# Optimization experiments

Hardware: AMD Instinct MI355X
Metric: run time of the kernel (lower is better)

## Reference

```python
import jax, jax.numpy as jnp
import numpy as np

IN_SIZE = 96
HIDDEN = 128
LIN_IN = 32
T = 65536


def setup_inputs() -> dict:
    key = jax.random.key(0)
    ks = jax.random.split(key, 6)
    s_ih = 1.0 / np.sqrt(HIDDEN)
    return {
        "input_GRU": jax.random.normal(ks[0], (T, IN_SIZE), dtype=jnp.float32),
        "input_linear": jax.random.normal(ks[1], (T, LIN_IN), dtype=jnp.float32),
        "init_hidden": jnp.zeros((HIDDEN,), dtype=jnp.float32),
        "w_ih": (jax.random.normal(ks[2], (3 * HIDDEN, IN_SIZE), dtype=jnp.float32) * s_ih),
        "w_hh": (jax.random.normal(ks[3], (3 * HIDDEN, HIDDEN), dtype=jnp.float32) * s_ih),
        "b_ih": (jax.random.normal(ks[4], (3 * HIDDEN,), dtype=jnp.float32) * s_ih),
        "b_n": (jax.random.normal(ks[5], (HIDDEN,), dtype=jnp.float32) * s_ih),
        "lin_bias": jnp.zeros((1,), dtype=jnp.float32),
    }


def reference(input_GRU, input_linear, init_hidden, w_ih, w_hh, b_ih, b_n, lin_bias):
    # Precompute all input-to-hidden projections as one big GEMM: (T, 3H)
    igates_all = input_GRU @ w_ih.T + b_ih

    def step(h, inp):
        igates, x_lin = inp
        hgates = w_hh @ h  # (3H,)
        ir, iz, in_ = jnp.split(igates, 3)
        hr, hz, hn = jnp.split(hgates, 3)
        r = jax.nn.sigmoid(ir + hr)  # reset gate
        z = jax.nn.sigmoid(iz + hz)  # update gate
        n = jnp.tanh(in_ + r * (hn + b_n))  # candidate
        h_new = n + z * (h - n)  # equinox GRUCell update
        # dynamic linear readout: first LIN_IN hidden units act as weight row
        out = jnp.dot(h_new[:LIN_IN], x_lin)[None] + lin_bias  # (1,)
        return h_new, out

    _, out = jax.lax.scan(step, init_hidden, (igates_all, input_linear))
    return out  # (T, 1)
```

## Files before the change

### kernel.cpp

```cpp
#include <hip/hip_runtime.h>
#include <math.h>

#define IN_SIZE 96
#define HID 128
#define H3 384
#define LIN_IN 32

__global__ __launch_bounds__(384, 2)
void igates_kernel(const float* __restrict__ x, const float* __restrict__ w_ih,
                   const float* __restrict__ b_ih, float* __restrict__ ig, int T)
{
    const int TT = 16;
    int t0 = blockIdx.x * TT;
    int j = threadIdx.x;
    __shared__ __align__(16) float xs[TT * IN_SIZE];
    for (int idx = j; idx < TT * IN_SIZE; idx += H3)
        xs[idx] = x[(size_t)t0 * IN_SIZE + idx];
    __syncthreads();

    float acc[TT];
    float b = b_ih[j];
#pragma unroll
    for (int tt = 0; tt < TT; tt++) acc[tt] = b;

    const float4* w4 = (const float4*)(w_ih + (size_t)j * IN_SIZE);
#pragma unroll
    for (int k = 0; k < IN_SIZE / 4; k++) {
        float4 wv = w4[k];
#pragma unroll
        for (int tt = 0; tt < TT; tt++) {
            const float4* xv4 = (const float4*)(xs + tt * IN_SIZE);
            float4 xv = xv4[k];
            acc[tt] = fmaf(wv.x, xv.x, acc[tt]);
            acc[tt] = fmaf(wv.y, xv.y, acc[tt]);
            acc[tt] = fmaf(wv.z, xv.z, acc[tt]);
            acc[tt] = fmaf(wv.w, xv.w, acc[tt]);
        }
    }
#pragma unroll
    for (int tt = 0; tt < TT; tt++)
        ig[(size_t)(t0 + tt) * H3 + j] = acc[tt];
}

__device__ __forceinline__ void fma4(float4& acc, const float4& wv, const float4& hv)
{
    acc.x = fmaf(wv.x, hv.x, acc.x);
    acc.y = fmaf(wv.y, hv.y, acc.y);
    acc.z = fmaf(wv.z, hv.z, acc.z);
    acc.w = fmaf(wv.w, hv.w, acc.w);
}

__device__ __forceinline__ float quad_sum(float x)
{
    float t;
    t = __int_as_float(__builtin_amdgcn_mov_dpp(__float_as_int(x), 0xB1, 0xF, 0xF, true));
    x += t;
    t = __int_as_float(__builtin_amdgcn_mov_dpp(__float_as_int(x), 0x4E, 0xF, 0xF, true));
    x += t;
    return x;
}

__device__ __forceinline__ void fast_barrier()
{
    asm volatile("s_waitcnt lgkmcnt(0)\n\ts_barrier" ::: "memory");
}

#define HPAD 36

__global__
__attribute__((amdgpu_flat_work_group_size(512, 512), amdgpu_waves_per_eu(2, 2)))
void scan_kernel(const float* __restrict__ ig, const float* __restrict__ h0,
                 const float* __restrict__ w_hh, const float* __restrict__ b_n,
                 float* __restrict__ hlin, int T)
{
    __shared__ __align__(16) float hs[4 * HPAD];

    const int tid = threadIdx.x;
    const int j = tid >> 2;
    const int kseg = tid & 3;
    const bool gate_lane = (kseg == 0);

    float4 w0[8], w1[8], w2[8];
    {
        const float* b0 = w_hh + (size_t)j * HID + kseg * 32;
        const float* b1 = w_hh + (size_t)(j + HID) * HID + kseg * 32;
        const float* b2 = w_hh + (size_t)(j + 2 * HID) * HID + kseg * 32;
#pragma unroll
        for (int k = 0; k < 8; k++) {
            w0[k] = ((const float4*)b0)[k];
            w1[k] = ((const float4*)b1)[k];
            w2[k] = ((const float4*)b2)[k];
        }
    }
    if (tid < HID) hs[(tid >> 5) * HPAD + (tid & 31)] = h0[tid];

    float bn = 0.f;
    float p00 = 0.f, p01 = 0.f, p02 = 0.f;
    float p10 = 0.f, p11 = 0.f, p12 = 0.f;
    if (gate_lane) {
        bn = b_n[j];
        p00 = ig[j];
        p01 = ig[HID + j];
        p02 = ig[2 * HID + j];
        const float* q = ig + H3;
        p10 = q[j];
        p11 = q[HID + j];
        p12 = q[2 * HID + j];
    }
    __syncthreads();

    const float4* hp = (const float4*)(hs + kseg * HPAD);
    const int hwidx = (j >> 5) * HPAD + (j & 31);

    const float* pf = ig + (size_t)2 * H3 + j;
    float* hl = hlin + j;

#define MATVEC_GATES(C0, C1, C2, DO_PREFETCH)                                  \
    {                                                                          \
        float4 a0 = {0.f, 0.f, 0.f, 0.f}, a1 = a0, a2 = a0;                    \
        _Pragma("unroll")                                                      \
        for (int kk = 0; kk < 8; kk++) {                                       \
            float4 hv = hp[kk];                                                \
            fma4(a0, w0[kk], hv);                                              \
            fma4(a1, w1[kk], hv);                                              \
            fma4(a2, w2[kk], hv);                                              \
        }                                                                      \
        float s0 = (a0.x + a0.y) + (a0.z + a0.w);                              \
        float s1 = (a1.x + a1.y) + (a1.z + a1.w);                              \
        float s2 = (a2.x + a2.y) + (a2.z + a2.w);                              \
        s0 = quad_sum(s0); s1 = quad_sum(s1); s2 = quad_sum(s2);               \
        if (gate_lane) {                                                       \
            float hprev = hs[hwidx];                                           \
            float er = __expf(-(C0 + s0));                                     \
            float r = __builtin_amdgcn_rcpf(1.f + er);                         \
            float ez = __expf(-(C1 + s1));                                     \
            float z = __builtin_amdgcn_rcpf(1.f + ez);                         \
            float xn = C2 + r * (s2 + bn);                                     \
            float e2 = __expf(-2.f * fabsf(xn));                               \
            float th = (1.f - e2) * __builtin_amdgcn_rcpf(1.f + e2);           \
            float nn = copysignf(th, xn);                                      \
            float hnew = nn + z * (hprev - nn);                                \
            hs[hwidx] = hnew;                                                  \
            if (j < LIN_IN) *hl = hnew;                                        \
            if (DO_PREFETCH) {                 \
                C0 = pf[0];                                                    \
                C1 = pf[HID];                                                  \
                C2 = pf[2 * HID];                                              \
            }                                                                  \
        }                                                                      \
        hl += LIN_IN;                                                          \
        pf += H3;                                                              \
        fast_barrier();                                                        \
    }

    int s = 0;
    for (; s + 4 <= T; s += 2) {
        MATVEC_GATES(p00, p01, p02, true)
        MATVEC_GATES(p10, p11, p12, true)
    }
    MATVEC_GATES(p00, p01, p02, false)
    MATVEC_GATES(p10, p11, p12, false)
#undef MATVEC_GATES
}

__global__ __launch_bounds__(256)
void readout_kernel(const float* __restrict__ hlin, const float* __restrict__ xlin,
                    const float* __restrict__ lbias, float* __restrict__ out, int T)
{
    int gid = blockIdx.x * 256 + threadIdx.x;
    int t = gid >> 3;
    int seg = gid & 7;
    if (t < T) {
        float4 hv = ((const float4*)hlin)[(size_t)t * 8 + seg];
        float4 xv = ((const float4*)xlin)[(size_t)t * 8 + seg];
        float p = hv.x * xv.x + hv.y * xv.y + hv.z * xv.z + hv.w * xv.w;
        p += __shfl_xor(p, 1);
        p += __shfl_xor(p, 2);
        p += __shfl_xor(p, 4);
        if (seg == 0) out[t] = p + lbias[0];
    }
}

extern "C" void kernel_launch(void* const* d_in, const int* in_sizes, int n_in,
                              void* d_out, int out_size, void* d_ws, size_t ws_size,
                              hipStream_t stream) {
    const float* x_gru = (const float*)d_in[0];
    const float* x_lin = (const float*)d_in[1];
    const float* h0    = (const float*)d_in[2];
    const float* w_ih  = (const float*)d_in[3];
    const float* w_hh  = (const float*)d_in[4];
    const float* b_ih  = (const float*)d_in[5];
    const float* b_n   = (const float*)d_in[6];
    const float* lbias = (const float*)d_in[7];
    float* out = (float*)d_out;

    int T = in_sizes[0] / IN_SIZE;
    float* igates = (float*)d_ws;
    float* hlin   = (float*)d_ws + (size_t)T * H3;

    igates_kernel<<<T / 16, 384, 0, stream>>>(x_gru, w_ih, b_ih, igates, T);
    scan_kernel<<<1, 512, 0, stream>>>(igates, h0, w_hh, b_n, hlin, T);
    readout_kernel<<<(T * 8 + 255) / 256, 256, 0, stream>>>(hlin, x_lin, lbias, out, T);
}
```

Baseline: 31.92 ms.

## Halve scan workgroup to 256 threads, each handling two hidden units

The sequential GRU scan now runs with 256 threads (4 waves) instead of 512. Each quad of threads computes gates for two hidden units (g and g+64), holding twice as many w_hh registers. The aim is to cut the per-step barrier cost and wave count on the serial critical path. In exchange each thread does twice the FMAs per step, and register pressure rises to 192 floats of weights per thread, which risks spills or a longer per-step latency.

```diff
diff --git a/kernel.cpp b/kernel.cpp
--- a/kernel.cpp
+++ b/kernel.cpp
@@ -65,10 +65,25 @@
     asm volatile("s_waitcnt lgkmcnt(0)\n\ts_barrier" ::: "memory");
 }
 
+__device__ __forceinline__ float gru_gate(float c0, float c1, float c2,
+                                          float s0, float s1, float s2,
+                                          float bn, float hprev)
+{
+    float er = __expf(-(c0 + s0));
+    float r = __builtin_amdgcn_rcpf(1.f + er);
+    float ez = __expf(-(c1 + s1));
+    float z = __builtin_amdgcn_rcpf(1.f + ez);
+    float xn = c2 + r * (s2 + bn);
+    float e2 = __expf(-2.f * fabsf(xn));
+    float th = (1.f - e2) * __builtin_amdgcn_rcpf(1.f + e2);
+    float nn = copysignf(th, xn);
+    return nn + z * (hprev - nn);
+}
+
 #define HPAD 36
 
 __global__
-__attribute__((amdgpu_flat_work_group_size(512, 512), amdgpu_waves_per_eu(2, 2)))
+__attribute__((amdgpu_flat_work_group_size(256, 256), amdgpu_waves_per_eu(1, 1)))
 void scan_kernel(const float* __restrict__ ig, const float* __restrict__ h0,
                  const float* __restrict__ w_hh, const float* __restrict__ b_n,
                  float* __restrict__ hlin, int T)
@@ -76,90 +91,106 @@
     __shared__ __align__(16) float hs[4 * HPAD];
 
     const int tid = threadIdx.x;
-    const int j = tid >> 2;
+    const int g = tid >> 2;
     const int kseg = tid & 3;
     const bool gate_lane = (kseg == 0);
 
-    float4 w0[8], w1[8], w2[8];
+    float4 wA0[8], wA1[8], wA2[8], wB0[8], wB1[8], wB2[8];
     {
-        const float* b0 = w_hh + (size_t)j * HID + kseg * 32;
-        const float* b1 = w_hh + (size_t)(j + HID) * HID + kseg * 32;
-        const float* b2 = w_hh + (size_t)(j + 2 * HID) * HID + kseg * 32;
+        const float* bA0 = w_hh + (size_t)g * HID + kseg * 32;
+        const float* bA1 = w_hh + (size_t)(g + HID) * HID + kseg * 32;
+        const float* bA2 = w_hh + (size_t)(g + 2 * HID) * HID + kseg * 32;
+        const float* bB0 = w_hh + (size_t)(g + 64) * HID + kseg * 32;
+        const float* bB1 = w_hh + (size_t)(g + 64 + HID) * HID + kseg * 32;
+        const float* bB2 = w_hh + (size_t)(g + 64 + 2 * HID) * HID + kseg * 32;
 #pragma unroll
         for (int k = 0; k < 8; k++) {
-            w0[k] = ((const float4*)b0)[k];
-            w1[k] = ((const float4*)b1)[k];
-            w2[k] = ((const float4*)b2)[k];
+            wA0[k] = ((const float4*)bA0)[k];
+            wA1[k] = ((const float4*)bA1)[k];
+            wA2[k] = ((const float4*)bA2)[k];
+            wB0[k] = ((const float4*)bB0)[k];
+            wB1[k] = ((const float4*)bB1)[k];
+            wB2[k] = ((const float4*)bB2)[k];
         }
     }
     if (tid < HID) hs[(tid >> 5) * HPAD + (tid & 31)] = h0[tid];
 
-    float bn = 0.f;
-    float p00 = 0.f, p01 = 0.f, p02 = 0.f;
-    float p10 = 0.f, p11 = 0.f, p12 = 0.f;
+    float bnA = 0.f, bnB = 0.f;
+    float pA00 = 0.f, pA01 = 0.f, pA02 = 0.f, pA10 = 0.f, pA11 = 0.f, pA12 = 0.f;
+    float pB00 = 0.f, pB01 = 0.f, pB02 = 0.f, pB10 = 0.f, pB11 = 0.f, pB12 = 0.f;
     if (gate_lane) {
-        bn = b_n[j];
-        p00 = ig[j];
-        p01 = ig[HID + j];
-        p02 = ig[2 * HID + j];
+        bnA = b_n[g];
+        bnB = b_n[g + 64];
+        pA00 = ig[g];            pB00 = ig[g + 64];
+        pA01 = ig[HID + g];      pB01 = ig[HID + g + 64];
+        pA02 = ig[2 * HID + g];  pB02 = ig[2 * HID + g + 64];
         const float* q = ig + H3;
-        p10 = q[j];
-        p11 = q[HID + j];
-        p12 = q[2 * HID + j];
+        pA10 = q[g];             pB10 = q[g + 64];
+        pA11 = q[HID + g];       pB11 = q[HID + g + 64];
+        pA12 = q[2 * HID + g];   pB12 = q[2 * HID + g + 64];
     }
     __syncthreads();
 
     const float4* hp = (const float4*)(hs + kseg * HPAD);
-    const int hwidx = (j >> 5) * HPAD + (j & 31);
-
-    const float* pf = ig + (size_t)2 * H3 + j;
-    float* hl = hlin + j;
-
-#define MATVEC_GATES(C0, C1, C2, DO_PREFETCH)                                  \
+    const int hwA = (g >> 5) * HPAD + (g & 31);
+    const int hwB = hwA + 2 * HPAD;
+
+    const float* pfA = ig + (size_t)2 * H3 + g;
+    const float* pfB = pfA + 64;
+    float* hl = hlin + g;
+
+#define MATVEC_GATES(A0, A1, A2, B0, B1, B2, DO_PREFETCH)                      \
     {                                                                          \
-        float4 a0 = {0.f, 0.f, 0.f, 0.f}, a1 = a0, a2 = a0;                    \
+        float hprevA = 0.f, hprevB = 0.f;                                      \
+        if (gate_lane) { hprevA = hs[hwA]; hprevB = hs[hwB]; }                 \
+        float4 aA0 = {0.f, 0.f, 0.f, 0.f}, aA1 = aA0, aA2 = aA0;               \
+        float4 aB0 = aA0, aB1 = aA0, aB2 = aA0;                                \
         _Pragma("unroll")                                                      \
         for (int kk = 0; kk < 8; kk++) {                                       \
             float4 hv = hp[kk];                                                \
-            fma4(a0, w0[kk], hv);                                              \
-            fma4(a1, w1[kk], hv);                                              \
-            fma4(a2, w2[kk], hv);                                              \
+            fma4(aA0, wA0[kk], hv);                                            \
+            fma4(aA1, wA1[kk], hv);                                            \
+            fma4(aA2, wA2[kk], hv);                                            \
+            fma4(aB0, wB0[kk], hv);                                            \
+            fma4(aB1, wB1[kk], hv);                                            \
+            fma4(aB2, wB2[kk], hv);                                            \
         }                                                                      \
-        float s0 = (a0.x + a0.y) + (a0.z + a0.w);                              \
-        float s1 = (a1.x + a1.y) + (a1.z + a1.w);                              \
-        float s2 = (a2.x + a2.y) + (a2.z + a2.w);                              \
-        s0 = quad_sum(s0); s1 = quad_sum(s1); s2 = quad_sum(s2);               \
+        float sA0 = (aA0.x + aA0.y) + (aA0.z + aA0.w);                         \
+        float sA1 = (aA1.x + aA1.y) + (aA1.z + aA1.w);                         \
+        float sA2 = (aA2.x + aA2.y) + (aA2.z + aA2.w);                         \
+        float sB0 = (aB0.x + aB0.y) + (aB0.z + aB0.w);                         \
+        float sB1 = (aB1.x + aB1.y) + (aB1.z + aB1.w);                         \
+        float sB2 = (aB2.x + aB2.y) + (aB2.z + aB2.w);                         \
+        sA0 = quad_sum(sA0); sA1 = quad_sum(sA1); sA2 = quad_sum(sA2);         \
+        sB0 = quad_sum(sB0); sB1 = quad_sum(sB1); sB2 = quad_sum(sB2);         \
         if (gate_lane) {                                                       \
-            float hprev = hs[hwidx];                                           \
-            float er = __expf(-(C0 + s0));                                     \
-            float r = __builtin_amdgcn_rcpf(1.f + er);                         \
-            float ez = __expf(-(C1 + s1));                                     \
-            float z = __builtin_amdgcn_rcpf(1.f + ez);                         \
-            float xn = C2 + r * (s2 + bn);                                     \
-            float e2 = __expf(-2.f * fabsf(xn));                               \
-            float th = (1.f - e2) * __builtin_amdgcn_rcpf(1.f + e2);           \
-            float nn = copysignf(th, xn);                                      \
-            float hnew = nn + z * (hprev - nn);                                \
-            hs[hwidx] = hnew;                                                  \
-            if (j < LIN_IN) *hl = hnew;                                        \
+            float hnewA = gru_gate(A0, A1, A2, sA0, sA1, sA2, bnA, hprevA);    \
+            float hnewB = gru_gate(B0, B1, B2, sB0, sB1, sB2, bnB, hprevB);    \
+            hs[hwA] = hnewA;                                                   \
+            hs[hwB] = hnewB;                                                   \
+            if (g < LIN_IN) *hl = hnewA;                                       \
             if (DO_PREFETCH) {                 \
-                C0 = pf[0];                                                    \
-                C1 = pf[HID];                                                  \
-                C2 = pf[2 * HID];                                              \
+                A0 = pfA[0];                                                   \
+                A1 = pfA[HID];                                                 \
+                A2 = pfA[2 * HID];                                             \
+                B0 = pfB[0];                                                   \
+                B1 = pfB[HID];                                                 \
+                B2 = pfB[2 * HID];                                             \
             }                                                                  \
         }                                                                      \
         hl += LIN_IN;                                                          \
-        pf += H3;                                                              \
+        pfA += H3;                                                             \
+        pfB += H3;                                                             \
         fast_barrier();                                                        \
     }
 
     int s = 0;
     for (; s + 4 <= T; s += 2) {
-        MATVEC_GATES(p00, p01, p02, true)
-        MATVEC_GATES(p10, p11, p12, true)
-    }
-    MATVEC_GATES(p00, p01, p02, false)
-    MATVEC_GATES(p10, p11, p12, false)
+        MATVEC_GATES(pA00, pA01, pA02, pB00, pB01, pB02, true)
+        MATVEC_GATES(pA10, pA11, pA12, pB10, pB11, pB12, true)
+    }
+    MATVEC_GATES(pA00, pA01, pA02, pB00, pB01, pB02, false)
+    MATVEC_GATES(pA10, pA11, pA12, pB10, pB11, pB12, false)
 #undef MATVEC_GATES
 }
 
@@ -199,6 +230,6 @@
     float* hlin   = (float*)d_ws + (size_t)T * H3;
 
     igates_kernel<<<T / 16, 384, 0, stream>>>(x_gru, w_ih, b_ih, igates, T);
-    scan_kernel<<<1, 512, 0, stream>>>(igates, h0, w_hh, b_n, hlin, T);
+    scan_kernel<<<1, 256, 0, stream>>>(igates, h0, w_hh, b_n, hlin, T);
     readout_kernel<<<(T * 8 + 255) / 256, 256, 0, stream>>>(hlin, x_lin, lbias, out, T);
 }
```

New measurement: 44.90 ms. +40.7%, slower.
